# Optimization experiments

Hardware: AMD Instinct MI355X
Metric: run time of the kernel (lower is better)

The kernel has to match this reference:

```python
import jax, jax.numpy as jnp
import numpy as np

N = 100000      # nodes
E = 3200000     # directed edges
F_IN = 128      # input node features
H = 16          # hidden width (fixed by module code)
C = 40          # classes
K_HOPS = 10
ALPHA = 0.1
BN_EPS = 1e-5


def gcn_conv(x, W, b, src, dst, n):
    """PyG GCNConv: add self-loops, symmetric D^-1/2 (A+I) D^-1/2 aggregation of x@W, plus bias."""
    loop = jnp.arange(n)
    s = jnp.concatenate([src, loop])
    d = jnp.concatenate([dst, loop])
    deg = jax.ops.segment_sum(jnp.ones(s.shape[0], x.dtype), d, num_segments=n)
    dinv = jnp.where(deg > 0, jax.lax.rsqrt(deg), 0.0)
    norm = dinv[s] * dinv[d]                      # [E+N]
    h = x @ W                                     # [N, out]
    out = jax.ops.segment_sum(h[s] * norm[:, None], d, num_segments=n)
    return out + b


def setup_inputs() -> dict:
    key = jax.random.key(0)
    ks = jax.random.split(key, 6)
    x = jax.random.normal(ks[0], (N, F_IN), jnp.float32)
    src = jax.random.randint(ks[1], (E,), 0, N)
    dst = jax.random.randint(ks[2], (E,), 0, N)
    glorot = lambda k, sh, fan: jax.random.normal(k, sh, jnp.float32) * np.float32(1.0 / np.sqrt(fan))
    W1 = glorot(ks[3], (F_IN, H), F_IN)
    b1 = jnp.zeros((H,), jnp.float32)
    gamma = jnp.ones((H,), jnp.float32)
    beta = jnp.zeros((H,), jnp.float32)
    Wl = glorot(ks[4], (H, H), H)
    bl = jnp.zeros((H,), jnp.float32)
    W2 = glorot(ks[5], (H, C), H)
    b2 = jnp.zeros((C,), jnp.float32)
    return dict(x=x, src=src, dst=dst, W1=W1, b1=b1, gamma=gamma, beta=beta,
                Wl=Wl, bl=bl, W2=W2, b2=b2)


def reference(x, src, dst, W1, b1, gamma, beta, Wl, bl, W2, b2):
    h = jax.nn.relu(gcn_conv(x, W1, b1, src, dst, N))
    # BatchNorm1d in training mode: biased batch statistics over nodes
    mean = h.mean(axis=0)
    var = h.var(axis=0)
    h = (h - mean) * jax.lax.rsqrt(var + BN_EPS) * gamma + beta
    # k_hops iterations of tiny linear-relu-residual blend
    def step(h, _):
        return ALPHA * jax.nn.relu(h @ Wl + bl) + (1.0 - ALPHA) * h, None
    h, _ = jax.lax.scan(step, h, None, length=K_HOPS)
    out = gcn_conv(h, W2, b2, src, dst, N)
    return jax.nn.log_softmax(out, axis=1)
```

## Files before the change

### kernel.cpp

```cpp
#include <hip/hip_runtime.h>
#include <hip/hip_fp16.h>
#include <math.h>

#define F_IN 128
#define H 16
#define C 40
#define K_HOPS 10
#define ALPHA 0.1f
#define BN_EPS 1e-5f

#define RB 256
#define RB_BITS 8
#define NBKT_MAX 512
#define SRC_MASK 0x1FFFF
#define PADQ 32
#define NDUMMY 2048
#define CAPB_BITS 14
#define CAPB (1 << CAPB_BITS)
#define STAGE_CAP 14336

typedef int v4i __attribute__((ext_vector_type(4)));

__global__ void k_zero(int* __restrict__ gcur, float* __restrict__ stats,
                       __half* __restrict__ h1h, __half* __restrict__ hh, int n) {
    int id = blockIdx.x * blockDim.x + threadIdx.x;
    if (id < NBKT_MAX) gcur[id] = id << CAPB_BITS;
    if (id < 32) stats[id] = 0.0f;
    int* z1 = (int*)(h1h + (size_t)n * H);
    int* z2 = (int*)(hh + (size_t)n * H);
    if (id < NDUMMY * H / 2) { z1[id] = 0; z2[id] = 0; }
}

#define BIN_CHUNK 4096
__global__ __launch_bounds__(512) void k_bin(const int* __restrict__ src,
                                             const int* __restrict__ dst,
                                             int* __restrict__ gcur,
                                             int* __restrict__ temp, int e) {
    __shared__ int hist[NBKT_MAX];
    __shared__ int cur[NBKT_MAX];
    __shared__ int gofs[NBKT_MAX];
    __shared__ int wsum[8];
    __shared__ int stageV[BIN_CHUNK];
    __shared__ int stageD[BIN_CHUNK];
    int t = threadIdx.x;
    hist[t] = 0;
    __syncthreads();
    int base = blockIdx.x * BIN_CHUNK;
    int cnt = e - base; if (cnt > BIN_CHUNK) cnt = BIN_CHUNK;
    const v4i* s4 = reinterpret_cast<const v4i*>(src + base);
    const v4i* d4 = reinterpret_cast<const v4i*>(dst + base);
    v4i sv[2], dv[2];
#pragma unroll
    for (int i = 0; i < 2; ++i) {
        int e0 = (t * 2 + i) * 4;
        if (e0 + 3 < cnt) { sv[i] = s4[t * 2 + i]; dv[i] = d4[t * 2 + i]; }
        else if (e0 < cnt) {
            int ts[4], td[4];
#pragma unroll
            for (int j = 0; j < 4; ++j) {
                int ei = e0 + j;
                ts[j] = (ei < cnt) ? src[base + ei] : 0;
                td[j] = (ei < cnt) ? dst[base + ei] : -1;
            }
            sv[i] = *reinterpret_cast<v4i*>(ts); dv[i] = *reinterpret_cast<v4i*>(td);
        } else { dv[i] = (v4i){-1, -1, -1, -1}; sv[i] = dv[i]; }
    }
#pragma unroll
    for (int i = 0; i < 2; ++i) {
        if (dv[i].x >= 0) atomicAdd(&hist[dv[i].x >> RB_BITS], 1);
        if (dv[i].y >= 0) atomicAdd(&hist[dv[i].y >> RB_BITS], 1);
        if (dv[i].z >= 0) atomicAdd(&hist[dv[i].z >> RB_BITS], 1);
        if (dv[i].w >= 0) atomicAdd(&hist[dv[i].w >> RB_BITS], 1);
    }
    __syncthreads();
    int v = hist[t];
    int lane = t & 63, wv = t >> 6;
    int s = v;
#pragma unroll
    for (int off = 1; off < 64; off <<= 1) { int u = __shfl_up(s, off); if (lane >= off) s += u; }
    if (lane == 63) wsum[wv] = s;
    __syncthreads();
    if (t < 8) {
        int x = wsum[t];
#pragma unroll
        for (int off = 1; off < 8; off <<= 1) { int u = __shfl_up(x, off); if (t >= off) x += u; }
        wsum[t] = x;
    }
    __syncthreads();
    int excl = s - v + (wv ? wsum[wv - 1] : 0);
    cur[t] = excl;
    int g = v ? atomicAdd(&gcur[t], v) : 0;
    gofs[t] = g - excl;
    __syncthreads();
#pragma unroll
    for (int i = 0; i < 2; ++i) {
        int ds[4] = { dv[i].x, dv[i].y, dv[i].z, dv[i].w };
        int ssx[4] = { sv[i].x, sv[i].y, sv[i].z, sv[i].w };
#pragma unroll
        for (int j = 0; j < 4; ++j) {
            int d = ds[j];
            if (d >= 0) {
                int b = d >> RB_BITS;
                int pos = atomicAdd(&cur[b], 1);
                stageV[pos] = ssx[j] | ((d & (RB - 1)) << 17);
                stageD[pos] = gofs[b];
            }
        }
    }
    __syncthreads();
    for (int i = t; i < cnt; i += 512)
        temp[stageD[i] + i] = stageV[i];
}

__global__ __launch_bounds__(256) void k_sort(const int* __restrict__ gcur,
                                              const int* __restrict__ temp,
                                              int* __restrict__ csr,
                                              int* __restrict__ ostart,
                                              int* __restrict__ oend,
                                              int* __restrict__ onode,
                                              float* __restrict__ dinv, int n) {
    __shared__ int hist[RB];
    __shared__ int cur[RB];
    __shared__ int wsum[8];
    __shared__ int qh[64];
    __shared__ int qb[64];
    __shared__ int ptotS;
    __shared__ int stage[STAGE_CAP];
    int t = threadIdx.x;
    int bkt = blockIdx.x;
    int start = bkt << CAPB_BITS;
    int endi = gcur[bkt];
    int nv = endi - start;
    int n4 = nv >> 2;
    const v4i* t4 = reinterpret_cast<const v4i*>(temp + start);
    hist[t] = 0;
    if (t < 64) qh[t] = 0;
    __syncthreads();
    for (int k = t; k < n4; k += 256) {
        v4i v = t4[k];
        atomicAdd(&hist[v.x >> 17], 1);
        atomicAdd(&hist[v.y >> 17], 1);
        atomicAdd(&hist[v.z >> 17], 1);
        atomicAdd(&hist[v.w >> 17], 1);
    }
    for (int k = start + (n4 << 2) + t; k < endi; k += 256)
        atomicAdd(&hist[temp[k] >> 17], 1);
    __syncthreads();
    int node = (bkt << RB_BITS) + t;
    int h = hist[t];
    int p = (h + PADQ - 1) & ~(PADQ - 1);
    bool va = (node < n);
    if (va) dinv[node] = rsqrtf((float)(h + 1));
    int lane = t & 63, wv = t >> 6;
    int s = p;
#pragma unroll
    for (int off = 1; off < 64; off <<= 1) { int u = __shfl_up(s, off); if (lane >= off) s += u; }
    if (lane == 63) wsum[wv] = s;
    __syncthreads();
    if (t < 4) {
        int x = wsum[t];
#pragma unroll
        for (int off = 1; off < 4; off <<= 1) { int u = __shfl_up(x, off); if (t >= off) x += u; }
        wsum[t] = x;
        if (t == 3) ptotS = x;
    }
    __syncthreads();
    int pexcl = s - p + (wv ? wsum[wv - 1] : 0);
    int s0 = start + pexcl;
    int q = 63 - min(p >> 5, 63);
    int r = atomicAdd(&qh[q], 1);
    __syncthreads();
    int ptotal = ptotS;
    if (t == 0) {
        int run = 0;
        for (int i = 0; i < 64; ++i) { qb[i] = run; run += qh[i]; }
    }
    __syncthreads();
    int ga = (bkt << RB_BITS) + qb[q] + r;
    ostart[ga] = s0; oend[ga] = s0 + p; onode[ga] = va ? node : -1;

    if (ptotal <= STAGE_CAP) {
        cur[t] = pexcl;
        for (int i = t; i < ptotal; i += 256) stage[i] = -1;
        __syncthreads();
        for (int k = t; k < n4; k += 256) {
            v4i v = t4[k];
            int p0 = atomicAdd(&cur[v.x >> 17], 1); stage[p0] = v.x & SRC_MASK;
            int p1 = atomicAdd(&cur[v.y >> 17], 1); stage[p1] = v.y & SRC_MASK;
            int p2 = atomicAdd(&cur[v.z >> 17], 1); stage[p2] = v.z & SRC_MASK;
            int p3 = atomicAdd(&cur[v.w >> 17], 1); stage[p3] = v.w & SRC_MASK;
        }
        for (int k = start + (n4 << 2) + t; k < endi; k += 256) {
            int v = temp[k];
            int pos = atomicAdd(&cur[v >> 17], 1);
            stage[pos] = v & SRC_MASK;
        }
        __syncthreads();
        for (int i = t * 4; i < ptotal; i += 1024) {
            v4i v = *reinterpret_cast<const v4i*>(&stage[i]);
            int gi = start + i;
            v.x = (v.x < 0) ? n + ((gi + 0) & (NDUMMY - 1)) : v.x;
            v.y = (v.y < 0) ? n + ((gi + 1) & (NDUMMY - 1)) : v.y;
            v.z = (v.z < 0) ? n + ((gi + 2) & (NDUMMY - 1)) : v.z;
            v.w = (v.w < 0) ? n + ((gi + 3) & (NDUMMY - 1)) : v.w;
            *reinterpret_cast<v4i*>(&csr[gi]) = v;
        }
    } else {
        cur[t] = s0;
        __syncthreads();
        for (int k = start + t; k < endi; k += 256) {
            int v = temp[k];
            int pos = atomicAdd(&cur[v >> 17], 1);
            csr[pos] = v & SRC_MASK;
        }
        __syncthreads();
        for (int i = s0 + h; i < s0 + p; ++i) csr[i] = n + (i & (NDUMMY - 1));
    }
}

__global__ __launch_bounds__(256) void k_mm1(const float* __restrict__ x,
                                             const float* __restrict__ W1,
                                             const float* __restrict__ dinv,
                                             __half* __restrict__ h1h, int n) {
    __shared__ __align__(16) float xs[16 * 132];
    __shared__ __align__(16) float ws[128 * 16];
    int t = threadIdx.x;
    int node0 = blockIdx.x * 16;
    const float4* x4 = reinterpret_cast<const float4*>(x);
    const float4* w4 = reinterpret_cast<const float4*>(W1);
#pragma unroll
    for (int r = 0; r < 2; ++r) {
        int f = t + r * 256;
        int nl = f >> 5, k4 = f & 31;
        int nn = node0 + nl; if (nn >= n) nn = n - 1;
        *reinterpret_cast<float4*>(&xs[nl * 132 + k4 * 4]) = x4[(size_t)nn * 32 + k4];
        *reinterpret_cast<float4*>(&ws[f * 4]) = w4[f];
    }
    __syncthreads();
    int nl = t >> 4, j = t & 15;
    float acc = 0.0f;
#pragma unroll 8
    for (int k = 0; k < 128; ++k)
        acc = fmaf(xs[nl * 132 + k], ws[k * 16 + j], acc);
    int node = node0 + nl;
    if (node < n) h1h[(size_t)node * H + j] = __float2half(acc * dinv[node]);
}

__device__ __forceinline__ void acc8(float* a, int4 gv) {
    const __half2* h = reinterpret_cast<const __half2*>(&gv);
    float2 f0 = __half22float2(h[0]);
    float2 f1 = __half22float2(h[1]);
    float2 f2 = __half22float2(h[2]);
    float2 f3 = __half22float2(h[3]);
    a[0] += f0.x; a[1] += f0.y; a[2] += f1.x; a[3] += f1.y;
    a[4] += f2.x; a[5] += f2.y; a[6] += f3.x; a[7] += f3.y;
}

__global__ __launch_bounds__(256) void k_gather1(const int* __restrict__ ostart,
                                                 const int* __restrict__ oend,
                                                 const int* __restrict__ onode,
                                                 const int* __restrict__ csr,
                                                 const __half* __restrict__ h1h,
                                                 const float* __restrict__ dinv,
                                                 const float* __restrict__ b1,
                                                 float* __restrict__ hout,
                                                 float* __restrict__ stats, int n) {
    __shared__ float sm[32];
    __shared__ float b1s[16];
    int t = threadIdx.x;
    if (t < 32) sm[t] = 0.0f;
    if (t < 16) b1s[t] = b1[t];
    __syncthreads();
    int idx = blockIdx.x * 256 + t;
    int g = idx >> 2;
    int L = idx & 3, p = L >> 1, jj = L & 1;
    int node = __builtin_nontemporal_load(onode + g);
    float a[8];
#pragma unroll
    for (int k = 0; k < 8; ++k) a[k] = 0.0f;
    const int4* tab = reinterpret_cast<const int4*>(h1h);
    if (node >= 0) {
        int c  = (__builtin_nontemporal_load(ostart + g) >> 2) + (p << 2);
        int ce = __builtin_nontemporal_load(oend + g) >> 2;
        const v4i* csr4 = reinterpret_cast<const v4i*>(csr);
        for (; c < ce; c += 8) {
            v4i e0 = __builtin_nontemporal_load(csr4 + c);
            v4i e1 = __builtin_nontemporal_load(csr4 + c + 1);
            v4i e2 = __builtin_nontemporal_load(csr4 + c + 2);
            v4i e3 = __builtin_nontemporal_load(csr4 + c + 3);
            int4 g0  = tab[(size_t)e0.x * 2 + jj];
            int4 g1  = tab[(size_t)e0.y * 2 + jj];
            int4 g2  = tab[(size_t)e0.z * 2 + jj];
            int4 g3  = tab[(size_t)e0.w * 2 + jj];
            int4 g4  = tab[(size_t)e1.x * 2 + jj];
            int4 g5  = tab[(size_t)e1.y * 2 + jj];
            int4 g6  = tab[(size_t)e1.z * 2 + jj];
            int4 g7  = tab[(size_t)e1.w * 2 + jj];
            int4 g8  = tab[(size_t)e2.x * 2 + jj];
            int4 g9  = tab[(size_t)e2.y * 2 + jj];
            int4 g10 = tab[(size_t)e2.z * 2 + jj];
            int4 g11 = tab[(size_t)e2.w * 2 + jj];
            int4 g12 = tab[(size_t)e3.x * 2 + jj];
            int4 g13 = tab[(size_t)e3.y * 2 + jj];
            int4 g14 = tab[(size_t)e3.z * 2 + jj];
            int4 g15 = tab[(size_t)e3.w * 2 + jj];
            acc8(a, g0);  acc8(a, g1);  acc8(a, g2);  acc8(a, g3);
            acc8(a, g4);  acc8(a, g5);  acc8(a, g6);  acc8(a, g7);
            acc8(a, g8);  acc8(a, g9);  acc8(a, g10); acc8(a, g11);
            acc8(a, g12); acc8(a, g13); acc8(a, g14); acc8(a, g15);
        }
    }
#pragma unroll
    for (int k = 0; k < 8; ++k) a[k] += __shfl_xor(a[k], 2);
    float din = 0.0f;
    int4 sv = make_int4(0, 0, 0, 0);
    if (node >= 0) {
        din = dinv[node];
        sv = tab[(size_t)node * 2 + jj];
    }
    float v[8];
    {
        const __half2* h = reinterpret_cast<const __half2*>(&sv);
        float2 f0 = __half22float2(h[0]), f1 = __half22float2(h[1]);
        float2 f2 = __half22float2(h[2]), f3 = __half22float2(h[3]);
        float s8[8] = { f0.x, f0.y, f1.x, f1.y, f2.x, f2.y, f3.x, f3.y };
        bool writer = (node >= 0) && (p == 0);
#pragma unroll
        for (int k = 0; k < 8; ++k) {
            float val = fmaxf(din * (a[k] + s8[k]) + b1s[jj * 8 + k], 0.0f);
            v[k] = writer ? val : 0.0f;
        }
        if (writer) {
            float4* o = reinterpret_cast<float4*>(hout + (size_t)node * H + jj * 8);
            o[0] = make_float4(v[0], v[1], v[2], v[3]);
            o[1] = make_float4(v[4], v[5], v[6], v[7]);
        }
    }
#pragma unroll
    for (int k = 0; k < 8; ++k) {
        float s1 = v[k], s2 = v[k] * v[k];
        s1 += __shfl_xor(s1, 2);  s2 += __shfl_xor(s2, 2);
        s1 += __shfl_xor(s1, 4);  s2 += __shfl_xor(s2, 4);
        s1 += __shfl_xor(s1, 8);  s2 += __shfl_xor(s2, 8);
        s1 += __shfl_xor(s1, 16); s2 += __shfl_xor(s2, 16);
        s1 += __shfl_xor(s1, 32); s2 += __shfl_xor(s2, 32);
        if ((t & 63) < 2) {
            atomicAdd(&sm[jj * 8 + k], s1);
            atomicAdd(&sm[16 + jj * 8 + k], s2);
        }
    }
    __syncthreads();
    if (t < 32) atomicAdd(&stats[t], sm[t]);
}

__global__ __launch_bounds__(256) void k_hops(const float* __restrict__ h,
                                              __half* __restrict__ hh,
                                              const float* __restrict__ stats,
                                              const float* __restrict__ gamma,
                                              const float* __restrict__ beta,
                                              const float* __restrict__ Wl,
                                              const float* __restrict__ bl,
                                              const float* __restrict__ dinv, int n, float nf) {
    __shared__ float wl[256], bls[16], av[16], cv[16];
    int t = threadIdx.x;
    wl[t] = Wl[(t & 15) * 16 + (t >> 4)];
    if (t < 16) {
        bls[t] = bl[t];
        float mean = stats[t] / nf;
        float var = stats[16 + t] / nf - mean * mean;
        float aa = gamma[t] * rsqrtf(var + BN_EPS);
        av[t] = aa;
        cv[t] = beta[t] - mean * aa;
    }
    __syncthreads();
    int node = blockIdx.x * 256 + t;
    if (node >= n) return;
    float hr[16];
    {
        const float4* hp = reinterpret_cast<const float4*>(h + (size_t)node * H);
        float4 v0 = hp[0], v1 = hp[1], v2 = hp[2], v3 = hp[3];
        hr[0] = v0.x; hr[1] = v0.y; hr[2] = v0.z; hr[3] = v0.w;
        hr[4] = v1.x; hr[5] = v1.y; hr[6] = v1.z; hr[7] = v1.w;
        hr[8] = v2.x; hr[9] = v2.y; hr[10] = v2.z; hr[11] = v2.w;
        hr[12] = v3.x; hr[13] = v3.y; hr[14] = v3.z; hr[15] = v3.w;
    }
#pragma unroll
    for (int j = 0; j < 16; ++j) hr[j] = hr[j] * av[j] + cv[j];
    for (int it = 0; it < K_HOPS; ++it) {
        float tmp[16];
#pragma unroll
        for (int j = 0; j < 16; ++j) {
            float a = bls[j];
#pragma unroll
            for (int k = 0; k < 16; ++k) a = fmaf(hr[k], wl[j * 16 + k], a);
            tmp[j] = fmaxf(a, 0.0f);
        }
#pragma unroll
        for (int j = 0; j < 16; ++j) hr[j] = ALPHA * tmp[j] + (1.0f - ALPHA) * hr[j];
    }
    {
        float din = dinv[node];
        __half2 ph[8];
#pragma unroll
        for (int i = 0; i < 8; ++i)
            ph[i] = __floats2half2_rn(hr[2 * i] * din, hr[2 * i + 1] * din);
        int4* hp = reinterpret_cast<int4*>(hh + (size_t)node * H);
        hp[0] = *reinterpret_cast<int4*>(&ph[0]);
        hp[1] = *reinterpret_cast<int4*>(&ph[4]);
    }
}

__global__ __launch_bounds__(256) void k_g2f(const int* __restrict__ ostart,
                                             const int* __restrict__ oend,
                                             const int* __restrict__ onode,
                                             const int* __restrict__ csr,
                                             const __half* __restrict__ hh,
                                             const float* __restrict__ dinv,
                                             const float* __restrict__ W2,
                                             const float* __restrict__ b2,
                                             float* __restrict__ out, int n) {
    __shared__ __align__(16) float w2t[40 * 20];
    __shared__ float b2s[40];
    __shared__ __align__(16) float feat[64 * 20];
    int t = threadIdx.x;
    for (int i = t; i < 640; i += 256) w2t[(i >> 4) * 20 + (i & 15)] = W2[(i & 15) * 40 + (i >> 4)];
    if (t < 40) b2s[t] = b2[t];
    int idx = blockIdx.x * 256 + t;
    int g = idx >> 2;
    int L = idx & 3, p = L >> 1, jj = L & 1;
    int node = __builtin_nontemporal_load(onode + g);
    float a[8];
#pragma unroll
    for (int k = 0; k < 8; ++k) a[k] = 0.0f;
    const int4* tab = reinterpret_cast<const int4*>(hh);
    if (node >= 0) {
        int c  = (__builtin_nontemporal_load(ostart + g) >> 2) + (p << 2);
        int ce = __builtin_nontemporal_load(oend + g) >> 2;
        const v4i* csr4 = reinterpret_cast<const v4i*>(csr);
        for (; c < ce; c += 8) {
            v4i e0 = __builtin_nontemporal_load(csr4 + c);
            v4i e1 = __builtin_nontemporal_load(csr4 + c + 1);
            v4i e2 = __builtin_nontemporal_load(csr4 + c + 2);
            v4i e3 = __builtin_nontemporal_load(csr4 + c + 3);
            int4 g0  = tab[(size_t)e0.x * 2 + jj];
            int4 g1  = tab[(size_t)e0.y * 2 + jj];
            int4 g2  = tab[(size_t)e0.z * 2 + jj];
            int4 g3  = tab[(size_t)e0.w * 2 + jj];
            int4 g4  = tab[(size_t)e1.x * 2 + jj];
            int4 g5  = tab[(size_t)e1.y * 2 + jj];
            int4 g6  = tab[(size_t)e1.z * 2 + jj];
            int4 g7  = tab[(size_t)e1.w * 2 + jj];
            int4 g8  = tab[(size_t)e2.x * 2 + jj];
            int4 g9  = tab[(size_t)e2.y * 2 + jj];
            int4 g10 = tab[(size_t)e2.z * 2 + jj];
            int4 g11 = tab[(size_t)e2.w * 2 + jj];
            int4 g12 = tab[(size_t)e3.x * 2 + jj];
            int4 g13 = tab[(size_t)e3.y * 2 + jj];
            int4 g14 = tab[(size_t)e3.z * 2 + jj];
            int4 g15 = tab[(size_t)e3.w * 2 + jj];
            acc8(a, g0);  acc8(a, g1);  acc8(a, g2);  acc8(a, g3);
            acc8(a, g4);  acc8(a, g5);  acc8(a, g6);  acc8(a, g7);
            acc8(a, g8);  acc8(a, g9);  acc8(a, g10); acc8(a, g11);
            acc8(a, g12); acc8(a, g13); acc8(a, g14); acc8(a, g15);
        }
    }
#pragma unroll
    for (int k = 0; k < 8; ++k) a[k] += __shfl_xor(a[k], 2);
    int nl = t >> 2;
    if (node >= 0 && p == 0) {
        float din = dinv[node];
        int4 sv = tab[(size_t)node * 2 + jj];
        const __half2* h = reinterpret_cast<const __half2*>(&sv);
        float2 f0 = __half22float2(h[0]), f1 = __half22float2(h[1]);
        float2 f2 = __half22float2(h[2]), f3 = __half22float2(h[3]);
        float s8[8] = { f0.x, f0.y, f1.x, f1.y, f2.x, f2.y, f3.x, f3.y };
        float v[8];
#pragma unroll
        for (int k = 0; k < 8; ++k) v[k] = din * (a[k] + s8[k]);
        *reinterpret_cast<float4*>(&feat[nl * 20 + jj * 8])     = make_float4(v[0], v[1], v[2], v[3]);
        *reinterpret_cast<float4*>(&feat[nl * 20 + jj * 8 + 4]) = make_float4(v[4], v[5], v[6], v[7]);
    }
    __syncthreads();
    float4 f0 = *reinterpret_cast<const float4*>(&feat[nl * 20]);
    float4 f1 = *reinterpret_cast<const float4*>(&feat[nl * 20 + 4]);
    float4 f2 = *reinterpret_cast<const float4*>(&feat[nl * 20 + 8]);
    float4 f3 = *reinterpret_cast<const float4*>(&feat[nl * 20 + 12]);
    int cb = (t & 3) * 10;
    float z[10];
#pragma unroll
    for (int j = 0; j < 10; ++j) {
        const float4* wr = reinterpret_cast<const float4*>(&w2t[(cb + j) * 20]);
        float4 w0 = wr[0], w1 = wr[1], w2v = wr[2], w3 = wr[3];
        float acc = b2s[cb + j];
        acc = fmaf(f0.x, w0.x, acc); acc = fmaf(f0.y, w0.y, acc);
        acc = fmaf(f0.z, w0.z, acc); acc = fmaf(f0.w, w0.w, acc);
        acc = fmaf(f1.x, w1.x, acc); acc = fmaf(f1.y, w1.y, acc);
        acc = fmaf(f1.z, w1.z, acc); acc = fmaf(f1.w, w1.w, acc);
        acc = fmaf(f2.x, w2v.x, acc); acc = fmaf(f2.y, w2v.y, acc);
        acc = fmaf(f2.z, w2v.z, acc); acc = fmaf(f2.w, w2v.w, acc);
        acc = fmaf(f3.x, w3.x, acc); acc = fmaf(f3.y, w3.y, acc);
        acc = fmaf(f3.z, w3.z, acc); acc = fmaf(f3.w, w3.w, acc);
        z[j] = acc;
    }
    float m = z[0];
#pragma unroll
    for (int j = 1; j < 10; ++j) m = fmaxf(m, z[j]);
    m = fmaxf(m, __shfl_xor(m, 1));
    m = fmaxf(m, __shfl_xor(m, 2));
    float s = 0.0f;
#pragma unroll
    for (int j = 0; j < 10; ++j) s += expf(z[j] - m);
    s += __shfl_xor(s, 1);
    s += __shfl_xor(s, 2);
    float lse = m + logf(s);
    if (node >= 0) {
        float2* o = reinterpret_cast<float2*>(out + (size_t)node * 40 + cb);
#pragma unroll
        for (int j = 0; j < 5; ++j)
            o[j] = make_float2(z[2 * j] - lse, z[2 * j + 1] - lse);
    }
}

extern "C" void kernel_launch(void* const* d_in, const int* in_sizes, int n_in,
                              void* d_out, int out_size, void* d_ws, size_t ws_size,
                              hipStream_t stream) {
    const float* x     = (const float*)d_in[0];
    const int*   src   = (const int*)d_in[1];
    const int*   dst   = (const int*)d_in[2];
    const float* W1    = (const float*)d_in[3];
    const float* b1    = (const float*)d_in[4];
    const float* gamma = (const float*)d_in[5];
    const float* beta  = (const float*)d_in[6];
    const float* Wl    = (const float*)d_in[7];
    const float* bl    = (const float*)d_in[8];
    const float* W2    = (const float*)d_in[9];
    const float* b2    = (const float*)d_in[10];
    float* out = (float*)d_out;

    int n = in_sizes[0] / F_IN;
    int e = in_sizes[1];
    int nbkt = (n + RB - 1) >> RB_BITS;
    int nAlign = (n + 15) & ~15;
    int nG = nbkt * RB;
    size_t bktB = (size_t)nbkt << CAPB_BITS;
    size_t hTileB = (size_t)nAlign * H * 4;
    size_t unionB = bktB * 4;
    if (unionB < hTileB) unionB = hTileB;

    char* wsb = (char*)d_ws;
    int*    csr      = (int*)wsb;      wsb += (bktB + 64) * 4;
    char*   uni      = wsb;            wsb += unionB;
    int*    temp     = (int*)uni;
    float*  hbuf     = (float*)uni;
    int*    ostart   = (int*)wsb;      wsb += (size_t)(nG + 16) * 4;
    int*    oend     = (int*)wsb;      wsb += (size_t)(nG + 16) * 4;
    int*    onode    = (int*)wsb;      wsb += (size_t)(nG + 16) * 4;
    float*  dinv     = (float*)wsb;    wsb += (size_t)nAlign * 4;
    int*    gcur     = (int*)wsb;      wsb += NBKT_MAX * 4;
    float*  stats    = (float*)wsb;    wsb += 64 * 4;
    __half* h1h      = (__half*)wsb;   wsb += (size_t)(nAlign + NDUMMY + 16) * H * 2;
    __half* hh       = (__half*)wsb;   wsb += (size_t)(nAlign + NDUMMY + 16) * H * 2;

    k_zero<<<64, 256, 0, stream>>>(gcur, stats, h1h, hh, n);
    k_bin<<<(e + BIN_CHUNK - 1) / BIN_CHUNK, 512, 0, stream>>>(src, dst, gcur, temp, e);
    k_sort<<<nbkt, 256, 0, stream>>>(gcur, temp, csr, ostart, oend, onode, dinv, n);
    k_mm1<<<(n + 15) / 16, 256, 0, stream>>>(x, W1, dinv, h1h, n);
    k_gather1<<<nbkt * 4, 256, 0, stream>>>(ostart, oend, onode, csr, h1h, dinv, b1, hbuf, stats, n);
    k_hops<<<(n + 255) / 256, 256, 0, stream>>>(hbuf, hh, stats, gamma, beta, Wl, bl, dinv, n, (float)n);
    k_g2f<<<nbkt * 4, 256, 0, stream>>>(ostart, oend, onode, csr, hh, dinv, W2, b2, out, n);
}
```

Measured before the change: 266.0 us.

## Halve CSR row padding to 16 and run sort with 512 threads

Node rows in the CSR are now padded to multiples of 16 instead of 32, which cuts the dummy-edge gathers that both aggregation kernels perform. The two gather kernels shrink their unrolled inner loop from 16 to 8 neighbours per lane pair so it matches the finer padding. The sort kernel now runs with 512 threads while keeping a 256-entry histogram, with guards on the per-node work. In exchange there are fewer loads in flight per iteration and more partially-useful loop trips.

```diff
diff --git a/kernel.cpp b/kernel.cpp
--- a/kernel.cpp
+++ b/kernel.cpp
@@ -13,7 +13,7 @@
 #define RB_BITS 8
 #define NBKT_MAX 512
 #define SRC_MASK 0x1FFFF
-#define PADQ 32
+#define PADQ 16
 #define NDUMMY 2048
 #define CAPB_BITS 14
 #define CAPB (1 << CAPB_BITS)
@@ -112,7 +112,7 @@
         temp[stageD[i] + i] = stageV[i];
 }
 
-__global__ __launch_bounds__(256) void k_sort(const int* __restrict__ gcur,
+__global__ __launch_bounds__(512) void k_sort(const int* __restrict__ gcur,
                                               const int* __restrict__ temp,
                                               int* __restrict__ csr,
                                               int* __restrict__ ostart,
@@ -121,7 +121,7 @@
                                               float* __restrict__ dinv, int n) {
     __shared__ int hist[RB];
     __shared__ int cur[RB];
-    __shared__ int wsum[8];
+    __shared__ int wsum[4];
     __shared__ int qh[64];
     __shared__ int qb[64];
     __shared__ int ptotS;
@@ -133,29 +133,33 @@
     int nv = endi - start;
     int n4 = nv >> 2;
     const v4i* t4 = reinterpret_cast<const v4i*>(temp + start);
-    hist[t] = 0;
+    if (t < RB) hist[t] = 0;
     if (t < 64) qh[t] = 0;
     __syncthreads();
-    for (int k = t; k < n4; k += 256) {
+    for (int k = t; k < n4; k += 512) {
         v4i v = t4[k];
         atomicAdd(&hist[v.x >> 17], 1);
         atomicAdd(&hist[v.y >> 17], 1);
         atomicAdd(&hist[v.z >> 17], 1);
         atomicAdd(&hist[v.w >> 17], 1);
     }
-    for (int k = start + (n4 << 2) + t; k < endi; k += 256)
+    for (int k = start + (n4 << 2) + t; k < endi; k += 512)
         atomicAdd(&hist[temp[k] >> 17], 1);
     __syncthreads();
     int node = (bkt << RB_BITS) + t;
-    int h = hist[t];
-    int p = (h + PADQ - 1) & ~(PADQ - 1);
-    bool va = (node < n);
-    if (va) dinv[node] = rsqrtf((float)(h + 1));
+    int h = 0, pv = 0;
+    bool va = false;
+    if (t < RB) {
+        h = hist[t];
+        pv = (h + PADQ - 1) & ~(PADQ - 1);
+        va = (node < n);
+        if (va) dinv[node] = rsqrtf((float)(h + 1));
+    }
     int lane = t & 63, wv = t >> 6;
-    int s = p;
+    int s = pv;
 #pragma unroll
     for (int off = 1; off < 64; off <<= 1) { int u = __shfl_up(s, off); if (lane >= off) s += u; }
-    if (lane == 63) wsum[wv] = s;
+    if (lane == 63 && wv < 4) wsum[wv] = s;
     __syncthreads();
     if (t < 4) {
         int x = wsum[t];
@@ -165,10 +169,13 @@
         if (t == 3) ptotS = x;
     }
     __syncthreads();
-    int pexcl = s - p + (wv ? wsum[wv - 1] : 0);
-    int s0 = start + pexcl;
-    int q = 63 - min(p >> 5, 63);
-    int r = atomicAdd(&qh[q], 1);
+    int pexcl = 0, s0 = 0, q = 63, r = 0;
+    if (t < RB) {
+        pexcl = s - pv + (wv ? wsum[wv - 1] : 0);
+        s0 = start + pexcl;
+        q = 63 - min(pv >> 4, 63);
+        r = atomicAdd(&qh[q], 1);
+    }
     __syncthreads();
     int ptotal = ptotS;
     if (t == 0) {
@@ -176,27 +183,28 @@
         for (int i = 0; i < 64; ++i) { qb[i] = run; run += qh[i]; }
     }
     __syncthreads();
-    int ga = (bkt << RB_BITS) + qb[q] + r;
-    ostart[ga] = s0; oend[ga] = s0 + p; onode[ga] = va ? node : -1;
-
+    if (t < RB) {
+        int ga = (bkt << RB_BITS) + qb[q] + r;
+        ostart[ga] = s0; oend[ga] = s0 + pv; onode[ga] = va ? node : -1;
+    }
     if (ptotal <= STAGE_CAP) {
-        cur[t] = pexcl;
-        for (int i = t; i < ptotal; i += 256) stage[i] = -1;
+        if (t < RB) cur[t] = pexcl;
+        for (int i = t; i < ptotal; i += 512) stage[i] = -1;
         __syncthreads();
-        for (int k = t; k < n4; k += 256) {
+        for (int k = t; k < n4; k += 512) {
             v4i v = t4[k];
             int p0 = atomicAdd(&cur[v.x >> 17], 1); stage[p0] = v.x & SRC_MASK;
             int p1 = atomicAdd(&cur[v.y >> 17], 1); stage[p1] = v.y & SRC_MASK;
             int p2 = atomicAdd(&cur[v.z >> 17], 1); stage[p2] = v.z & SRC_MASK;
             int p3 = atomicAdd(&cur[v.w >> 17], 1); stage[p3] = v.w & SRC_MASK;
         }
-        for (int k = start + (n4 << 2) + t; k < endi; k += 256) {
+        for (int k = start + (n4 << 2) + t; k < endi; k += 512) {
             int v = temp[k];
             int pos = atomicAdd(&cur[v >> 17], 1);
             stage[pos] = v & SRC_MASK;
         }
         __syncthreads();
-        for (int i = t * 4; i < ptotal; i += 1024) {
+        for (int i = t * 4; i < ptotal; i += 2048) {
             v4i v = *reinterpret_cast<const v4i*>(&stage[i]);
             int gi = start + i;
             v.x = (v.x < 0) ? n + ((gi + 0) & (NDUMMY - 1)) : v.x;
@@ -206,15 +214,15 @@
             *reinterpret_cast<v4i*>(&csr[gi]) = v;
         }
     } else {
-        cur[t] = s0;
+        if (t < RB) cur[t] = s0;
         __syncthreads();
-        for (int k = start + t; k < endi; k += 256) {
+        for (int k = start + t; k < endi; k += 512) {
             int v = temp[k];
             int pos = atomicAdd(&cur[v >> 17], 1);
             csr[pos] = v & SRC_MASK;
         }
         __syncthreads();
-        for (int i = s0 + h; i < s0 + p; ++i) csr[i] = n + (i & (NDUMMY - 1));
+        if (t < RB) for (int i = s0 + h; i < s0 + pv; ++i) csr[i] = n + (i & (NDUMMY - 1));
     }
 }
 
@@ -280,34 +288,22 @@
     for (int k = 0; k < 8; ++k) a[k] = 0.0f;
     const int4* tab = reinterpret_cast<const int4*>(h1h);
     if (node >= 0) {
-        int c  = (__builtin_nontemporal_load(ostart + g) >> 2) + (p << 2);
+        int c  = (__builtin_nontemporal_load(ostart + g) >> 2) + (p << 1);
         int ce = __builtin_nontemporal_load(oend + g) >> 2;
         const v4i* csr4 = reinterpret_cast<const v4i*>(csr);
-        for (; c < ce; c += 8) {
+        for (; c < ce; c += 4) {
             v4i e0 = __builtin_nontemporal_load(csr4 + c);
             v4i e1 = __builtin_nontemporal_load(csr4 + c + 1);
-            v4i e2 = __builtin_nontemporal_load(csr4 + c + 2);
-            v4i e3 = __builtin_nontemporal_load(csr4 + c + 3);
-            int4 g0  = tab[(size_t)e0.x * 2 + jj];
-            int4 g1  = tab[(size_t)e0.y * 2 + jj];
-            int4 g2  = tab[(size_t)e0.z * 2 + jj];
-            int4 g3  = tab[(size_t)e0.w * 2 + jj];
-            int4 g4  = tab[(size_t)e1.x * 2 + jj];
-            int4 g5  = tab[(size_t)e1.y * 2 + jj];
-            int4 g6  = tab[(size_t)e1.z * 2 + jj];
-            int4 g7  = tab[(size_t)e1.w * 2 + jj];
-            int4 g8  = tab[(size_t)e2.x * 2 + jj];
-            int4 g9  = tab[(size_t)e2.y * 2 + jj];
-            int4 g10 = tab[(size_t)e2.z * 2 + jj];
-            int4 g11 = tab[(size_t)e2.w * 2 + jj];
-            int4 g12 = tab[(size_t)e3.x * 2 + jj];
-            int4 g13 = tab[(size_t)e3.y * 2 + jj];
-            int4 g14 = tab[(size_t)e3.z * 2 + jj];
-            int4 g15 = tab[(size_t)e3.w * 2 + jj];
-            acc8(a, g0);  acc8(a, g1);  acc8(a, g2);  acc8(a, g3);
-            acc8(a, g4);  acc8(a, g5);  acc8(a, g6);  acc8(a, g7);
-            acc8(a, g8);  acc8(a, g9);  acc8(a, g10); acc8(a, g11);
-            acc8(a, g12); acc8(a, g13); acc8(a, g14); acc8(a, g15);
+            int4 g0 = tab[(size_t)e0.x * 2 + jj];
+            int4 g1 = tab[(size_t)e0.y * 2 + jj];
+            int4 g2 = tab[(size_t)e0.z * 2 + jj];
+            int4 g3 = tab[(size_t)e0.w * 2 + jj];
+            int4 g4 = tab[(size_t)e1.x * 2 + jj];
+            int4 g5 = tab[(size_t)e1.y * 2 + jj];
+            int4 g6 = tab[(size_t)e1.z * 2 + jj];
+            int4 g7 = tab[(size_t)e1.w * 2 + jj];
+            acc8(a, g0); acc8(a, g1); acc8(a, g2); acc8(a, g3);
+            acc8(a, g4); acc8(a, g5); acc8(a, g6); acc8(a, g7);
         }
     }
 #pragma unroll
@@ -434,34 +430,22 @@
     for (int k = 0; k < 8; ++k) a[k] = 0.0f;
     const int4* tab = reinterpret_cast<const int4*>(hh);
     if (node >= 0) {
-        int c  = (__builtin_nontemporal_load(ostart + g) >> 2) + (p << 2);
+        int c  = (__builtin_nontemporal_load(ostart + g) >> 2) + (p << 1);
         int ce = __builtin_nontemporal_load(oend + g) >> 2;
         const v4i* csr4 = reinterpret_cast<const v4i*>(csr);
-        for (; c < ce; c += 8) {
+        for (; c < ce; c += 4) {
             v4i e0 = __builtin_nontemporal_load(csr4 + c);
             v4i e1 = __builtin_nontemporal_load(csr4 + c + 1);
-            v4i e2 = __builtin_nontemporal_load(csr4 + c + 2);
-            v4i e3 = __builtin_nontemporal_load(csr4 + c + 3);
-            int4 g0  = tab[(size_t)e0.x * 2 + jj];
-            int4 g1  = tab[(size_t)e0.y * 2 + jj];
-            int4 g2  = tab[(size_t)e0.z * 2 + jj];
-            int4 g3  = tab[(size_t)e0.w * 2 + jj];
-            int4 g4  = tab[(size_t)e1.x * 2 + jj];
-            int4 g5  = tab[(size_t)e1.y * 2 + jj];
-            int4 g6  = tab[(size_t)e1.z * 2 + jj];
-            int4 g7  = tab[(size_t)e1.w * 2 + jj];
-            int4 g8  = tab[(size_t)e2.x * 2 + jj];
-            int4 g9  = tab[(size_t)e2.y * 2 + jj];
-            int4 g10 = tab[(size_t)e2.z * 2 + jj];
-            int4 g11 = tab[(size_t)e2.w * 2 + jj];
-            int4 g12 = tab[(size_t)e3.x * 2 + jj];
-            int4 g13 = tab[(size_t)e3.y * 2 + jj];
-            int4 g14 = tab[(size_t)e3.z * 2 + jj];
-            int4 g15 = tab[(size_t)e3.w * 2 + jj];
-            acc8(a, g0);  acc8(a, g1);  acc8(a, g2);  acc8(a, g3);
-            acc8(a, g4);  acc8(a, g5);  acc8(a, g6);  acc8(a, g7);
-            acc8(a, g8);  acc8(a, g9);  acc8(a, g10); acc8(a, g11);
-            acc8(a, g12); acc8(a, g13); acc8(a, g14); acc8(a, g15);
+            int4 g0 = tab[(size_t)e0.x * 2 + jj];
+            int4 g1 = tab[(size_t)e0.y * 2 + jj];
+            int4 g2 = tab[(size_t)e0.z * 2 + jj];
+            int4 g3 = tab[(size_t)e0.w * 2 + jj];
+            int4 g4 = tab[(size_t)e1.x * 2 + jj];
+            int4 g5 = tab[(size_t)e1.y * 2 + jj];
+            int4 g6 = tab[(size_t)e1.z * 2 + jj];
+            int4 g7 = tab[(size_t)e1.w * 2 + jj];
+            acc8(a, g0); acc8(a, g1); acc8(a, g2); acc8(a, g3);
+            acc8(a, g4); acc8(a, g5); acc8(a, g6); acc8(a, g7);
         }
     }
 #pragma unroll
@@ -563,7 +547,7 @@
 
     k_zero<<<64, 256, 0, stream>>>(gcur, stats, h1h, hh, n);
     k_bin<<<(e + BIN_CHUNK - 1) / BIN_CHUNK, 512, 0, stream>>>(src, dst, gcur, temp, e);
-    k_sort<<<nbkt, 256, 0, stream>>>(gcur, temp, csr, ostart, oend, onode, dinv, n);
+    k_sort<<<nbkt, 512, 0, stream>>>(gcur, temp, csr, ostart, oend, onode, dinv, n);
     k_mm1<<<(n + 15) / 16, 256, 0, stream>>>(x, W1, dinv, h1h, n);
     k_gather1<<<nbkt * 4, 256, 0, stream>>>(ostart, oend, onode, csr, h1h, dinv, b1, hbuf, stats, n);
     k_hops<<<(n + 255) / 256, 256, 0, stream>>>(hbuf, hh, stats, gamma, beta, Wl, bl, dinv, n, (float)n);
```

Measured after the change: 261.1 us. About the same (-1.8%).
